# Performance work log

Hardware: AMD Instinct MI355X
Metric: run time of the kernel (lower is better)

Reference implementation:

```python
import jax, jax.numpy as jnp
import numpy as np

OUT, IN = 4096, 4096
GROUP_SIZE = 64
NUM_GROUPS = IN // GROUP_SIZE  # 64


def dequantize(packed, mn, scale):
    # packed: [OUT, NUM_GROUPS, GROUP_SIZE//2] int32, byte values 0..255.
    # 4-bit asymmetric layout (torch compress): high nibble holds the first
    # half of each group, low nibble the second half.
    hi = (packed >> 4) & 0xF                      # [OUT, G, 32]
    lo = packed & 0xF                             # [OUT, G, 32]
    vals = jnp.concatenate([hi, lo], axis=-1).astype(jnp.float32)  # [OUT, G, 64]
    w = vals / scale + mn                         # scale, mn broadcast [OUT, G, 1]
    return w.reshape(OUT, IN)


def setup_inputs() -> dict:
    key = jax.random.key(0)
    k1, k2, k3, k4, k5 = jax.random.split(key, 5)
    x = jax.random.normal(k1, (4, 2048, IN), dtype=jnp.float32)
    packed = jax.random.randint(k2, (OUT, NUM_GROUPS, GROUP_SIZE // 2), 0, 256, dtype=jnp.int32)
    mn = jax.random.normal(k3, (OUT, NUM_GROUPS, 1), dtype=jnp.float32) * 0.02
    # scale = B / (mx - mn) is positive; keep it away from zero.
    scale = jax.random.uniform(k4, (OUT, NUM_GROUPS, 1), dtype=jnp.float32) * 200.0 + 100.0
    bias = jax.random.normal(k5, (OUT,), dtype=jnp.float32) * 0.02
    return {"x": x, "packed": packed, "mn": mn, "scale": scale, "bias": bias}


def reference(x, packed, mn, scale, bias):
    w = dequantize(packed, mn, scale)             # [OUT, IN] fp32
    # F.linear: out = x @ w.T + bias
    return jnp.einsum('bsk,nk->bsn', x, w) + bias
```

## Files before the change

kernel.cpp:

```cpp
#include <hip/hip_runtime.h>

typedef unsigned short u16;
typedef __bf16 bf16x8 __attribute__((ext_vector_type(8)));
typedef float f32x4 __attribute__((ext_vector_type(4)));

#define M_DIM 8192
#define N_DIM 4096
#define K_DIM 4096

__device__ __forceinline__ u16 f2bf(float f) {
  unsigned int u = __float_as_uint(f);
  u += 0x7fffu + ((u >> 16) & 1u);
  return (u16)(u >> 16);
}

#define DQ_BLOCKS 32768
__global__ __launch_bounds__(256) void prep_kernel(
    const int* __restrict__ packed, const float* __restrict__ mn,
    const float* __restrict__ scale, u16* __restrict__ W,
    const float4* __restrict__ x, ushort4* __restrict__ xb) {
  int b = blockIdx.x;
  if (b < DQ_BLOCKS) {
    int idx = b * 256 + threadIdx.x;
    int j = idx & 31;
    int g = (idx >> 5) & 63;
    int n = idx >> 11;
    int p = packed[idx];
    float inv = 1.0f / scale[(n << 6) + g];
    float m = mn[(n << 6) + g];
    float hi = (float)((p >> 4) & 0xF) * inv + m;
    float lo = (float)(p & 0xF) * inv + m;
    int base = (n << 12) + (g << 6) + j;
    W[base] = f2bf(hi);
    W[base + 32] = f2bf(lo);
  } else {
    int i = (b - DQ_BLOCKS) * 256 + threadIdx.x;
    float4 a = x[i];
    ushort4 o;
    o.x = f2bf(a.x); o.y = f2bf(a.y); o.z = f2bf(a.z); o.w = f2bf(a.w);
    xb[i] = o;
  }
}

__device__ __forceinline__ void gload_lds16(const u16* g, u16* l) {
  __builtin_amdgcn_global_load_lds(
      (const __attribute__((address_space(1))) void*)g,
      (__attribute__((address_space(3))) void*)l, 16, 0, 0);
}

__global__ __launch_bounds__(256) void gemm_kernel(
    const u16* __restrict__ A,
    const u16* __restrict__ B,
    const float* __restrict__ bias,
    float* __restrict__ C) {
  __shared__ alignas(16) u16 As[2 * 128 * 32];
  __shared__ alignas(16) u16 Bs[2 * 128 * 32];

  const int tid = threadIdx.x;
  const int wave = tid >> 6;
  const int lane = tid & 63;
  const int lr = lane & 15;
  const int lq = lane >> 4;

  const int bn = blockIdx.x & 31;
  const int bm = blockIdx.x >> 5;
  const int m0 = bm << 7;
  const int n0 = bn << 7;

  const int wm = (wave & 1) << 6;
  const int wn = (wave >> 1) << 6;

  const int off0 = (wave << 10) + (lane << 4);
  const int srow = off0 >> 6;
  const int scol = (off0 & 63) >> 1;

  const u16* gA = A + (size_t)(m0 + srow) * K_DIM + scol;
  const u16* gB = B + (size_t)(n0 + srow) * K_DIM + scol;
  u16* ldsA0 = As + (wave << 9);
  u16* ldsB0 = Bs + (wave << 9);

  f32x4 acc[4][4] = {};

  for (int k0 = 0; k0 < K_DIM; k0 += 64) {
    gload_lds16(gA + k0, ldsA0);
    gload_lds16(gA + (size_t)64 * K_DIM + k0, ldsA0 + 2048);
    gload_lds16(gB + k0, ldsB0);
    gload_lds16(gB + (size_t)64 * K_DIM + k0, ldsB0 + 2048);
    gload_lds16(gA + k0 + 32, ldsA0 + 4096);
    gload_lds16(gA + (size_t)64 * K_DIM + k0 + 32, ldsA0 + 6144);
    gload_lds16(gB + k0 + 32, ldsB0 + 4096);
    gload_lds16(gB + (size_t)64 * K_DIM + k0 + 32, ldsB0 + 6144);
    __syncthreads();

#pragma unroll
    for (int s = 0; s < 2; s++) {
      const u16* as = As + s * 4096;
      const u16* bs = Bs + s * 4096;
      bf16x8 af[4], bfr[4];
#pragma unroll
      for (int i = 0; i < 4; i++)
        af[i] = *(const bf16x8*)(as + (wm + i * 16 + lr) * 32 + lq * 8);
#pragma unroll
      for (int j = 0; j < 4; j++)
        bfr[j] = *(const bf16x8*)(bs + (wn + j * 16 + lr) * 32 + lq * 8);
#pragma unroll
      for (int i = 0; i < 4; i++)
#pragma unroll
        for (int j = 0; j < 4; j++)
          acc[i][j] = __builtin_amdgcn_mfma_f32_16x16x32_bf16(
              af[i], bfr[j], acc[i][j], 0, 0, 0);
    }
    __syncthreads();
  }

#pragma unroll
  for (int j = 0; j < 4; j++) {
    int n = n0 + wn + j * 16 + lr;
    float bv = bias[n];
#pragma unroll
    for (int i = 0; i < 4; i++) {
      int mb = m0 + wm + i * 16 + lq * 4;
#pragma unroll
      for (int t = 0; t < 4; t++)
        C[(size_t)(mb + t) * N_DIM + n] = acc[i][j][t] + bv;
    }
  }
}

__global__ __launch_bounds__(256) void fallback_gemm(
    const float* __restrict__ x, const int* __restrict__ packed,
    const float* __restrict__ mn, const float* __restrict__ scale,
    const float* __restrict__ bias, float* __restrict__ out) {
  __shared__ float As[16][17];
  __shared__ float Bs[16][17];
  int tx = threadIdx.x & 15, ty = threadIdx.x >> 4;
  int m = blockIdx.y * 16 + ty;
  int n = blockIdx.x * 16 + tx;
  float acc = 0.f;
  for (int k0 = 0; k0 < K_DIM; k0 += 16) {
    As[ty][tx] = x[(size_t)m * K_DIM + k0 + tx];
    int nn = blockIdx.x * 16 + ty;
    int k = k0 + tx;
    int g = k >> 6, pos = k & 63;
    int p = packed[nn * 2048 + g * 32 + (pos & 31)];
    int v = (pos < 32) ? ((p >> 4) & 0xF) : (p & 0xF);
    Bs[ty][tx] = (float)v / scale[nn * 64 + g] + mn[nn * 64 + g];
    __syncthreads();
#pragma unroll
    for (int kk = 0; kk < 16; kk++) acc += As[ty][kk] * Bs[tx][kk];
    __syncthreads();
  }
  out[(size_t)m * N_DIM + n] = acc + bias[n];
}

extern "C" void kernel_launch(void* const* d_in, const int* in_sizes, int n_in,
                              void* d_out, int out_size, void* d_ws, size_t ws_size,
                              hipStream_t stream) {
  const float* x = (const float*)d_in[0];
  const int* packed = (const int*)d_in[1];
  const float* mn = (const float*)d_in[2];
  const float* scale = (const float*)d_in[3];
  const float* bias = (const float*)d_in[4];
  float* out = (float*)d_out;

  const size_t needW = (size_t)N_DIM * K_DIM * 2;
  const size_t needX = (size_t)M_DIM * K_DIM * 2;

  if (ws_size >= needW + needX) {
    u16* W = (u16*)d_ws;
    u16* Xb = (u16*)((char*)d_ws + needW);
    const int cvt_blocks = (int)((size_t)M_DIM * K_DIM / 4 / 256);
    prep_kernel<<<DQ_BLOCKS + cvt_blocks, 256, 0, stream>>>(
        packed, mn, scale, W, (const float4*)x, (ushort4*)Xb);
    gemm_kernel<<<(M_DIM / 128) * (N_DIM / 128), 256, 0, stream>>>(Xb, W, bias,
                                                                   out);
  } else {
    dim3 grid(N_DIM / 16, M_DIM / 16);
    fallback_gemm<<<grid, 256, 0, stream>>>(x, packed, mn, scale, bias, out);
  }
}
```

Baseline: 529.2 us.

## Dequantize int4 weights inside GEMM with fp16 MFMA and 256x128 tiles

The full bf16 weight matrix is no longer materialized. Weights are repacked to 4-bit words and dequantized in registers inside the GEMM using an fp16 magic-number trick, with a packed inverse-scale and offset table. Activations become fp16 instead of bf16, and the block tile grows to 256x128 with 8x4 accumulators per wave, which improves A reuse. The aim is to cut weight write and read traffic and prep cost. In exchange it adds per-iteration ALU dequant work, more register pressure, and fp16 precision risk from the round-toward-zero conversion of x.

```diff
diff --git a/kernel.cpp b/kernel.cpp
--- a/kernel.cpp
+++ b/kernel.cpp
@@ -1,114 +1,158 @@
 #include <hip/hip_runtime.h>
 
 typedef unsigned short u16;
-typedef __bf16 bf16x8 __attribute__((ext_vector_type(8)));
+typedef unsigned int u32;
+typedef _Float16 f16;
+typedef f16 f16x2 __attribute__((ext_vector_type(2)));
+typedef f16 f16x8 __attribute__((ext_vector_type(8)));
+typedef __fp16 h16x2 __attribute__((ext_vector_type(2)));
 typedef float f32x4 __attribute__((ext_vector_type(4)));
 
 #define M_DIM 8192
 #define N_DIM 4096
 #define K_DIM 4096
 
-__device__ __forceinline__ u16 f2bf(float f) {
-  unsigned int u = __float_as_uint(f);
-  u += 0x7fffu + ((u >> 16) & 1u);
-  return (u16)(u >> 16);
-}
-
-#define DQ_BLOCKS 32768
+#define XCVT_BLOCKS 16384
+#define W4_BLOCKS 8192
+#define IM_BLOCKS 1024
+
 __global__ __launch_bounds__(256) void prep_kernel(
-    const int* __restrict__ packed, const float* __restrict__ mn,
-    const float* __restrict__ scale, u16* __restrict__ W,
-    const float4* __restrict__ x, ushort4* __restrict__ xb) {
+    const float4* __restrict__ x, uint4* __restrict__ xh,
+    const int* __restrict__ packed, u32* __restrict__ w4,
+    const float* __restrict__ mn, const float* __restrict__ scale,
+    uint2* __restrict__ invmn) {
   int b = blockIdx.x;
-  if (b < DQ_BLOCKS) {
-    int idx = b * 256 + threadIdx.x;
-    int j = idx & 31;
-    int g = (idx >> 5) & 63;
-    int n = idx >> 11;
-    int p = packed[idx];
-    float inv = 1.0f / scale[(n << 6) + g];
-    float m = mn[(n << 6) + g];
-    float hi = (float)((p >> 4) & 0xF) * inv + m;
-    float lo = (float)(p & 0xF) * inv + m;
-    int base = (n << 12) + (g << 6) + j;
-    W[base] = f2bf(hi);
-    W[base + 32] = f2bf(lo);
+  if (b < XCVT_BLOCKS) {
+    int i = b * 256 + threadIdx.x;
+    float4 a0 = x[2 * i], a1 = x[2 * i + 1];
+    h16x2 h0 = __builtin_amdgcn_cvt_pkrtz(a0.x, a0.y);
+    h16x2 h1 = __builtin_amdgcn_cvt_pkrtz(a0.z, a0.w);
+    h16x2 h2 = __builtin_amdgcn_cvt_pkrtz(a1.x, a1.y);
+    h16x2 h3 = __builtin_amdgcn_cvt_pkrtz(a1.z, a1.w);
+    uint4 o;
+    o.x = __builtin_bit_cast(u32, h0);
+    o.y = __builtin_bit_cast(u32, h1);
+    o.z = __builtin_bit_cast(u32, h2);
+    o.w = __builtin_bit_cast(u32, h3);
+    xh[i] = o;
+  } else if (b < XCVT_BLOCKS + W4_BLOCKS) {
+    int idx = (b - XCVT_BLOCKS) * 256 + threadIdx.x;
+    int n = idx >> 9, w = idx & 511;
+    int g = w >> 3;
+    int jb = (w & 7) << 3;
+    int sh = (jb < 32) ? 4 : 0;
+    const int* p = packed + n * 2048 + g * 32 + (jb & 31);
+    u32 out = 0;
+#pragma unroll
+    for (int t = 0; t < 8; t++) {
+      u32 nib = ((u32)p[t] >> sh) & 0xFu;
+      int pos = ((t & 1) ? 16 : 0) + ((t >> 1) << 2);
+      out |= nib << pos;
+    }
+    w4[idx] = out;
   } else {
-    int i = (b - DQ_BLOCKS) * 256 + threadIdx.x;
-    float4 a = x[i];
-    ushort4 o;
-    o.x = f2bf(a.x); o.y = f2bf(a.y); o.z = f2bf(a.z); o.w = f2bf(a.w);
-    xb[i] = o;
-  }
-}
-
-__device__ __forceinline__ void gload_lds16(const u16* g, u16* l) {
+    int idx = (b - XCVT_BLOCKS - W4_BLOCKS) * 256 + threadIdx.x;
+    int n = idx & 4095, g = idx >> 12;
+    float sc = scale[n * 64 + g];
+    float m = mn[n * 64 + g];
+    f16 invh = (f16)(1.0f / sc);
+    f16 mnh = (f16)(m - 16.0f * (float)invh);
+    u32 ib = (u32)__builtin_bit_cast(u16, invh);
+    u32 mb = (u32)__builtin_bit_cast(u16, mnh);
+    uint2 o;
+    o.x = ib | (ib << 16);
+    o.y = mb | (mb << 16);
+    invmn[idx] = o;
+  }
+}
+
+__device__ __forceinline__ void gload_lds16(const void* g, void* l) {
   __builtin_amdgcn_global_load_lds(
       (const __attribute__((address_space(1))) void*)g,
       (__attribute__((address_space(3))) void*)l, 16, 0, 0);
 }
 
-__global__ __launch_bounds__(256) void gemm_kernel(
+__global__ __launch_bounds__(256, 2) void gemm4_kernel(
     const u16* __restrict__ A,
-    const u16* __restrict__ B,
-    const float* __restrict__ bias,
-    float* __restrict__ C) {
-  __shared__ alignas(16) u16 As[2 * 128 * 32];
-  __shared__ alignas(16) u16 Bs[2 * 128 * 32];
+    const u32* __restrict__ B4,
+    const uint2* __restrict__ IM,
+    const float* __restrict__ bias, float* __restrict__ C) {
+  __shared__ alignas(16) u16 As[2][256 * 32];
+  __shared__ alignas(16) u32 Bs[2][128 * 4];
 
   const int tid = threadIdx.x;
-  const int wave = tid >> 6;
-  const int lane = tid & 63;
-  const int lr = lane & 15;
-  const int lq = lane >> 4;
-
-  const int bn = blockIdx.x & 31;
-  const int bm = blockIdx.x >> 5;
-  const int m0 = bm << 7;
-  const int n0 = bn << 7;
-
-  const int wm = (wave & 1) << 6;
-  const int wn = (wave >> 1) << 6;
-
-  const int off0 = (wave << 10) + (lane << 4);
-  const int srow = off0 >> 6;
-  const int scol = (off0 & 63) >> 1;
-
-  const u16* gA = A + (size_t)(m0 + srow) * K_DIM + scol;
-  const u16* gB = B + (size_t)(n0 + srow) * K_DIM + scol;
-  u16* ldsA0 = As + (wave << 9);
-  u16* ldsB0 = Bs + (wave << 9);
-
-  f32x4 acc[4][4] = {};
-
-  for (int k0 = 0; k0 < K_DIM; k0 += 64) {
-    gload_lds16(gA + k0, ldsA0);
-    gload_lds16(gA + (size_t)64 * K_DIM + k0, ldsA0 + 2048);
-    gload_lds16(gB + k0, ldsB0);
-    gload_lds16(gB + (size_t)64 * K_DIM + k0, ldsB0 + 2048);
-    gload_lds16(gA + k0 + 32, ldsA0 + 4096);
-    gload_lds16(gA + (size_t)64 * K_DIM + k0 + 32, ldsA0 + 6144);
-    gload_lds16(gB + k0 + 32, ldsB0 + 4096);
-    gload_lds16(gB + (size_t)64 * K_DIM + k0 + 32, ldsB0 + 6144);
+  const int wave = tid >> 6, lane = tid & 63;
+  const int lr = lane & 15, lq = lane >> 4;
+  const int bn = blockIdx.x & 31, bm = blockIdx.x >> 5;
+  const int m0 = bm << 8, n0 = bn << 7;
+  const int wm = (wave & 1) << 7, wn = (wave >> 1) << 6;
+
+  const u16* pA =
+      A + (size_t)(m0 + (wave << 6) + (lane >> 2)) * K_DIM + ((lane & 3) << 3);
+  char* dstA = (char*)(&As[0][0]) + wave * 4096 + lane * 16;
+  const u32* pB = B4 + (size_t)(n0 + ((wave & 1) << 6) + lane) * 512 +
+                  ((wave >> 1) << 2);
+  char* dstB = (char*)(&Bs[0][0]) + wave * 1024 + lane * 16;
+  const uint2* pI = IM + n0 + wn + lr;
+
+  f32x4 acc[8][4] = {};
+
+  for (int kk = 0; kk < 64; ++kk) {
+    uint2 im[4];
+    const uint2* pIt = pI + kk * 4096;
+#pragma unroll
+    for (int j = 0; j < 4; j++) im[j] = pIt[j * 16];
+
+#pragma unroll
+    for (int s = 0; s < 2; s++)
+#pragma unroll
+      for (int c = 0; c < 4; c++)
+        gload_lds16(pA + kk * 64 + s * 32 + (size_t)c * 16 * K_DIM,
+                    dstA + s * 16384 + c * 1024);
+    gload_lds16(pB + kk * 8, dstB);
     __syncthreads();
 
 #pragma unroll
     for (int s = 0; s < 2; s++) {
-      const u16* as = As + s * 4096;
-      const u16* bs = Bs + s * 4096;
-      bf16x8 af[4], bfr[4];
-#pragma unroll
-      for (int i = 0; i < 4; i++)
-        af[i] = *(const bf16x8*)(as + (wm + i * 16 + lr) * 32 + lq * 8);
-#pragma unroll
-      for (int j = 0; j < 4; j++)
-        bfr[j] = *(const bf16x8*)(bs + (wn + j * 16 + lr) * 32 + lq * 8);
-#pragma unroll
-      for (int i = 0; i < 4; i++)
+      f16x8 af[8];
+#pragma unroll
+      for (int i = 0; i < 8; i++)
+        af[i] = *(const f16x8*)((const char*)(&As[0][0]) + s * 16384 +
+                                (wm + i * 16 + lr) * 64 + lq * 16);
+      u32 braw[4];
+#pragma unroll
+      for (int j = 0; j < 4; j++) braw[j] = Bs[s][(wn + j * 16 + lr) * 4 + lq];
+
+      f16x8 bf[4];
+#pragma unroll
+      for (int j = 0; j < 4; j++) {
+        u32 d = braw[j];
+        u32 q0 = ((d << 6) & 0x03C003C0u) | 0x4C004C00u;
+        u32 q1 = ((d << 2) & 0x03C003C0u) | 0x4C004C00u;
+        u32 q2 = ((d >> 2) & 0x03C003C0u) | 0x4C004C00u;
+        u32 q3 = ((d >> 6) & 0x03C003C0u) | 0x4C004C00u;
+        f16x2 inv2 = __builtin_bit_cast(f16x2, im[j].x);
+        f16x2 mn2 = __builtin_bit_cast(f16x2, im[j].y);
+        f16x2 w0 = __builtin_elementwise_fma(__builtin_bit_cast(f16x2, q0), inv2, mn2);
+        f16x2 w1 = __builtin_elementwise_fma(__builtin_bit_cast(f16x2, q1), inv2, mn2);
+        f16x2 w2 = __builtin_elementwise_fma(__builtin_bit_cast(f16x2, q2), inv2, mn2);
+        f16x2 w3 = __builtin_elementwise_fma(__builtin_bit_cast(f16x2, q3), inv2, mn2);
+        union {
+          f16x8 v;
+          u32 d[4];
+        } u;
+        u.d[0] = __builtin_bit_cast(u32, w0);
+        u.d[1] = __builtin_bit_cast(u32, w1);
+        u.d[2] = __builtin_bit_cast(u32, w2);
+        u.d[3] = __builtin_bit_cast(u32, w3);
+        bf[j] = u.v;
+      }
+#pragma unroll
+      for (int i = 0; i < 8; i++)
 #pragma unroll
         for (int j = 0; j < 4; j++)
-          acc[i][j] = __builtin_amdgcn_mfma_f32_16x16x32_bf16(
-              af[i], bfr[j], acc[i][j], 0, 0, 0);
+          acc[i][j] = __builtin_amdgcn_mfma_f32_16x16x32_f16(af[i], bf[j],
+                                                             acc[i][j], 0, 0, 0);
     }
     __syncthreads();
   }
@@ -118,8 +162,8 @@
     int n = n0 + wn + j * 16 + lr;
     float bv = bias[n];
 #pragma unroll
-    for (int i = 0; i < 4; i++) {
-      int mb = m0 + wm + i * 16 + lq * 4;
+    for (int i = 0; i < 8; i++) {
+      int mb = m0 + wm + i * 16 + (lq << 2);
 #pragma unroll
       for (int t = 0; t < 4; t++)
         C[(size_t)(mb + t) * N_DIM + n] = acc[i][j][t] + bv;
@@ -154,8 +198,8 @@
 }
 
 extern "C" void kernel_launch(void* const* d_in, const int* in_sizes, int n_in,
-                              void* d_out, int out_size, void* d_ws, size_t ws_size,
-                              hipStream_t stream) {
+                              void* d_out, int out_size, void* d_ws,
+                              size_t ws_size, hipStream_t stream) {
   const float* x = (const float*)d_in[0];
   const int* packed = (const int*)d_in[1];
   const float* mn = (const float*)d_in[2];
@@ -163,17 +207,18 @@
   const float* bias = (const float*)d_in[4];
   float* out = (float*)d_out;
 
-  const size_t needW = (size_t)N_DIM * K_DIM * 2;
-  const size_t needX = (size_t)M_DIM * K_DIM * 2;
-
-  if (ws_size >= needW + needX) {
-    u16* W = (u16*)d_ws;
-    u16* Xb = (u16*)((char*)d_ws + needW);
-    const int cvt_blocks = (int)((size_t)M_DIM * K_DIM / 4 / 256);
-    prep_kernel<<<DQ_BLOCKS + cvt_blocks, 256, 0, stream>>>(
-        packed, mn, scale, W, (const float4*)x, (ushort4*)Xb);
-    gemm_kernel<<<(M_DIM / 128) * (N_DIM / 128), 256, 0, stream>>>(Xb, W, bias,
-                                                                   out);
+  const size_t offW4 = (size_t)M_DIM * K_DIM * 2;
+  const size_t offIM = offW4 + (size_t)N_DIM * K_DIM / 2;
+  const size_t need = offIM + (size_t)64 * N_DIM * 8;
+
+  if (ws_size >= need) {
+    u16* Xh = (u16*)d_ws;
+    u32* W4 = (u32*)((char*)d_ws + offW4);
+    uint2* IMp = (uint2*)((char*)d_ws + offIM);
+    prep_kernel<<<XCVT_BLOCKS + W4_BLOCKS + IM_BLOCKS, 256, 0, stream>>>(
+        (const float4*)x, (uint4*)Xh, packed, W4, mn, scale, IMp);
+    gemm4_kernel<<<(M_DIM / 256) * (N_DIM / 128), 256, 0, stream>>>(
+        Xh, W4, IMp, bias, out);
   } else {
     dim3 grid(N_DIM / 16, M_DIM / 16);
     fallback_gemm<<<grid, 256, 0, stream>>>(x, packed, mn, scale, bias, out);
```

After: 513.0 us. 1.03x faster.
